# Kernel optimization log

Hardware: AMD Instinct MI355X
Metric: run time of the kernel (lower is better)

## Reference

```python
import jax, jax.numpy as jnp
import numpy as np

FILTER_K = 10      # per-class top-K support retention
TAU = 1.0          # temperature
SCALE = 20.0       # prototype logit scale
EPS = 1e-12


def _normalize(x, axis=-1):
    n = jnp.linalg.norm(x, axis=axis, keepdims=True)
    return x / jnp.maximum(n, EPS)


def _entropy(logits):
    p = jax.nn.softmax(logits, axis=1)
    return -(p * jax.nn.log_softmax(logits, axis=1)).sum(axis=1)


def _quantile(x, q):
    # linear-interpolation quantile (matches torch.quantile default)
    s = jnp.sort(x)
    n = x.shape[0]
    pos = q * (n - 1)
    lo = jnp.floor(pos).astype(jnp.int32)
    hi = jnp.minimum(lo + 1, n - 1)
    frac = pos - lo.astype(x.dtype)
    return s[lo] * (1.0 - frac) + s[hi] * frac


def setup_inputs() -> dict:
    key = jax.random.key(0)
    k1, k2, k3, k4, k5 = jax.random.split(key, 5)
    B, D, C = 65536, 512, 50
    feat = jax.random.normal(k1, (B, D), jnp.float32)
    logits_raw = jax.random.normal(k2, (B, C), jnp.float32)
    logits_aug = jax.random.normal(k3, (B, C), jnp.float32)
    W = jax.random.normal(k4, (C, D), jnp.float32) * 0.05  # classifier weight
    b = jax.random.normal(k5, (C,), jnp.float32) * 0.05    # classifier bias
    return {"feat": feat, "logits_raw": logits_raw, "logits_aug": logits_aug, "W": W, "b": b}


def reference(feat, logits_raw, logits_aug, W, b):
    C, D = W.shape
    # --- warmup memory initialized from classifier weights (as in __init__) ---
    wl = W @ W.T + b                       # (C, C)
    p0 = jax.nn.softmax(wl, axis=1)
    lab0 = jnp.argmax(wl, axis=1)          # (C,)
    ent0 = _entropy(wl)
    conf0 = p0.max(axis=1)

    # --- online batch stats ---
    logits = feat @ W.T + b                # (B, C)
    p = jax.nn.softmax(logits, axis=1)
    yhat = jnp.argmax(logits, axis=1)
    ent = _entropy(logits)
    pmax = p.max(axis=1)

    # dynamic entropy-quantile threshold (ent_thresh=None path)
    m = ent.mean()
    dyn_q = jnp.where(m >= 0.45, 0.25, jnp.where(m >= 0.38, 0.3, 0.4))
    thr = _quantile(ent, dyn_q)
    mask = ent <= thr
    # dual-view consistency gate
    mask &= jnp.argmax(logits_raw, axis=1) == jnp.argmax(logits_aug, axis=1)
    # confidence gate
    conf_thr = jnp.where(m >= 0.45, 0.72, 0.62)
    mask &= pmax >= conf_thr

    # --- grown support memory (warmup + accepted batch samples), static shape + valid mask ---
    supports = jnp.concatenate([W, feat], axis=0)          # (C+B, D)
    lab_idx = jnp.concatenate([lab0, yhat], axis=0)        # (C+B,)
    ents = jnp.concatenate([ent0, ent], axis=0)
    conf = jnp.concatenate([conf0, pmax], axis=0)
    valid = jnp.concatenate([jnp.ones((C,), bool), mask], axis=0)

    # --- per-class top-K lowest-entropy pruning (vectorized over classes) ---
    cls_mask = (lab_idx[None, :] == jnp.arange(C)[:, None]) & valid[None, :]  # (C, C+B)
    masked_ent = jnp.where(cls_mask, ents[None, :], jnp.inf)
    order = jnp.argsort(masked_ent, axis=1)
    ranks = jnp.argsort(order, axis=1)                     # rank of each entry within its class
    keep = (cls_mask & (ranks < FILTER_K)).any(axis=0)     # (C+B,)

    # --- confidence-weighted centroids + cosine-sim classification ---
    S = _normalize(supports)
    onehot = jax.nn.one_hot(lab_idx, C, dtype=supports.dtype)
    lab_w = onehot * jnp.maximum(conf, 1e-6)[:, None] * keep[:, None].astype(supports.dtype)
    denom = jnp.maximum(lab_w.sum(axis=0, keepdims=True), EPS)
    centroids = _normalize((lab_w / denom).T @ S)          # (C, D)
    sim = _normalize(feat) @ centroids.T                   # (B, C)
    return SCALE * sim / max(TAU, 1e-6)
```

## Files before the change

### kernel.cpp

```cpp
#include <hip/hip_runtime.h>
#include <math.h>

constexpr int BN = 65536;
constexpr int DK = 512;
constexpr int CN = 50;
constexpr int FILTK = 10;
constexpr int BR = 64;
constexpr int KC = 32;
constexpr int AS = 36;
constexpr int BS = 68;
constexpr int SELB = 64;

constexpr int W_SC     = 0;
constexpr int W_H1     = 64;
constexpr int W_H2LO   = 2112;
constexpr int W_H2HI   = 4160;
constexpr int W_H3LO   = 6208;
constexpr int W_H3HI   = 7232;
constexpr int ZERO_WORDS = 8256;
constexpr int W_ENT    = ZERO_WORDS;
constexpr int W_PMAX   = W_ENT  + BN;
constexpr int W_YHAT   = W_PMAX + BN;
constexpr int W_CONS   = W_YHAT + BN;
constexpr int W_NORM   = W_CONS + BN;
constexpr int W_LAB0   = W_NORM + BN;
constexpr int W_ENT0   = W_LAB0 + 64;
constexpr int W_CONF0  = W_ENT0 + 64;
constexpr int W_WNORM  = W_CONF0 + 64;
constexpr int LE_CAP   = BN + 64;
constexpr int W_LECLS  = W_WNORM + 64;
constexpr int W_LEENT  = W_LECLS  + LE_CAP;
constexpr int W_LECONF = W_LEENT  + LE_CAP;
constexpr int W_LEORD  = W_LECONF + LE_CAP;
constexpr int W_LESRC  = W_LEORD  + LE_CAP;
constexpr int W_LEW    = W_LESRC  + LE_CAP;
constexpr int W_CENT   = W_LEW    + LE_CAP;

struct Scalars {
    float    sum_ent;
    float    mean;
    float    conf_thr;
    float    frac;
    int      klo;
    int      khi;
    unsigned prefix_lo;
    unsigned rank_lo;
    unsigned prefix_hi;
    unsigned rank_hi;
    float    thr;
    unsigned cnt;
    unsigned done1, done2, done3;
};

__device__ __forceinline__ unsigned fkey(float f) {
    unsigned u = __float_as_uint(f);
    return (u & 0x80000000u) ? ~u : (u | 0x80000000u);
}
__device__ __forceinline__ float funkey(unsigned u) {
    return (u & 0x80000000u) ? __uint_as_float(u & 0x7fffffffu) : __uint_as_float(~u);
}

__global__ void init_kernel(const float* __restrict__ W, const float* __restrict__ bias,
                            int* __restrict__ lab0, float* __restrict__ ent0,
                            float* __restrict__ conf0, float* __restrict__ wnorm,
                            unsigned* __restrict__ wsz) {
    if (blockIdx.x >= CN) {
        for (int i = (blockIdx.x - CN) * 64 + threadIdx.x; i < ZERO_WORDS; i += 128)
            wsz[i] = 0u;
        return;
    }
    __shared__ float wrow[DK];
    const int i = blockIdx.x, l = threadIdx.x;
    float4 v0 = *(const float4*)(W + i * DK + l * 4);
    float4 v1 = *(const float4*)(W + i * DK + 256 + l * 4);
    *(float4*)(wrow + l * 4) = v0;
    *(float4*)(wrow + 256 + l * 4) = v1;
    float sq = v0.x*v0.x + v0.y*v0.y + v0.z*v0.z + v0.w*v0.w
             + v1.x*v1.x + v1.y*v1.y + v1.z*v1.z + v1.w*v1.w;
    #pragma unroll
    for (int m = 1; m < 64; m <<= 1) sq += __shfl_xor(sq, m);
    if (l == 0) wnorm[i] = sqrtf(sq);
    __syncthreads();

    float dot = -INFINITY;
    int   ai  = 0x7fffffff;
    if (l < CN) {
        const float* wj = W + l * DK;
        float d2 = 0.f;
        for (int d = 0; d < DK; d += 4) {
            float4 a  = *(const float4*)(wrow + d);
            float4 b4 = *(const float4*)(wj + d);
            d2 = fmaf(a.x, b4.x, fmaf(a.y, b4.y, fmaf(a.z, b4.z, fmaf(a.w, b4.w, d2))));
        }
        dot = d2 + bias[l];
        ai  = l;
    }
    float mx = dot; int am = ai;
    #pragma unroll
    for (int m = 32; m >= 1; m >>= 1) {
        float o = __shfl_xor(mx, m); int oi = __shfl_xor(am, m);
        if (o > mx || (o == mx && oi < am)) { mx = o; am = oi; }
    }
    float e = 0.f, te = 0.f;
    if (l < CN) { e = expf(dot - mx); te = e * (dot - mx); }
    #pragma unroll
    for (int m = 1; m < 64; m <<= 1) { e += __shfl_xor(e, m); te += __shfl_xor(te, m); }
    if (l == 0) {
        lab0[i]  = am;
        ent0[i]  = logf(e) - te / e;
        conf0[i] = 1.f / e;
    }
}

template <int MODE>
__global__ __launch_bounds__(256) void gemm_kernel(
        const float* __restrict__ A, const float* __restrict__ Bm,
        const float* __restrict__ bias,
        float* __restrict__ ent, float* __restrict__ pmaxA,
        int* __restrict__ yhat, float* __restrict__ rnorm,
        const float* __restrict__ in_norm, float* __restrict__ outp,
        const float* __restrict__ lraw, const float* __restrict__ laug,
        unsigned* __restrict__ consp, Scalars* sc) {
    __shared__ float smem[BR * AS + KC * BS];
    float* Af = smem;
    float* Bw = smem + BR * AS;
    const int t = threadIdx.x;
    const int tx = t & 15, ty = t >> 4;
    const int row0 = blockIdx.x * BR;
    const int srow = t >> 3, sf4 = t & 7;

    if (MODE == 0 && t < BR) {
        int r = row0 + t;
        const float* rp = lraw + r * CN;
        const float* ap = laug + r * CN;
        float m1 = rp[0]; int a1 = 0;
        float m2 = ap[0]; int a2 = 0;
        for (int j = 1; j < CN; j++) {
            float v1 = rp[j]; if (v1 > m1) { m1 = v1; a1 = j; }
            float v2 = ap[j]; if (v2 > m2) { m2 = v2; a2 = j; }
        }
        consp[r] = (a1 == a2) ? 1u : 0u;
    }

    float acc[4][4];
    #pragma unroll
    for (int q = 0; q < 4; q++)
        #pragma unroll
        for (int p = 0; p < 4; p++) acc[q][p] = 0.f;
    float sq0 = 0.f, sq1 = 0.f;

    for (int k0 = 0; k0 < DK; k0 += KC) {
        __syncthreads();
        float4 va0 = *(const float4*)(A + (row0 + srow) * DK + k0 + sf4 * 4);
        float4 va1 = *(const float4*)(A + (row0 + srow + 32) * DK + k0 + sf4 * 4);
        *(float4*)(Af + srow * AS + sf4 * 4) = va0;
        *(float4*)(Af + (srow + 32) * AS + sf4 * 4) = va1;
        if (MODE == 0) {
            sq0 += va0.x*va0.x + va0.y*va0.y + va0.z*va0.z + va0.w*va0.w;
            sq1 += va1.x*va1.x + va1.y*va1.y + va1.z*va1.z + va1.w*va1.w;
        }
        #pragma unroll
        for (int h = 0; h < 2; h++) {
            int c = (t >> 3) + h * 32;
            float4 vb = make_float4(0.f, 0.f, 0.f, 0.f);
            if (c < CN) vb = *(const float4*)(Bm + c * DK + k0 + sf4 * 4);
            Bw[(sf4 * 4 + 0) * BS + c] = vb.x;
            Bw[(sf4 * 4 + 1) * BS + c] = vb.y;
            Bw[(sf4 * 4 + 2) * BS + c] = vb.z;
            Bw[(sf4 * 4 + 3) * BS + c] = vb.w;
        }
        __syncthreads();
        #pragma unroll
        for (int kk = 0; kk < KC; kk += 4) {
            float4 a[4], bb[4];
            #pragma unroll
            for (int q = 0; q < 4; q++) a[q] = *(const float4*)(Af + (ty * 4 + q) * AS + kk);
            #pragma unroll
            for (int j = 0; j < 4; j++) bb[j] = *(const float4*)(Bw + (kk + j) * BS + tx * 4);
            #pragma unroll
            for (int q = 0; q < 4; q++) {
                float aq[4] = {a[q].x, a[q].y, a[q].z, a[q].w};
                #pragma unroll
                for (int j = 0; j < 4; j++) {
                    acc[q][0] = fmaf(aq[j], bb[j].x, acc[q][0]);
                    acc[q][1] = fmaf(aq[j], bb[j].y, acc[q][1]);
                    acc[q][2] = fmaf(aq[j], bb[j].z, acc[q][2]);
                    acc[q][3] = fmaf(aq[j], bb[j].w, acc[q][3]);
                }
            }
        }
    }

    if (MODE == 0) {
        float s0 = sq0, s1 = sq1;
        #pragma unroll
        for (int m = 1; m < 8; m <<= 1) { s0 += __shfl_xor(s0, m); s1 += __shfl_xor(s1, m); }
        if (sf4 == 0) { rnorm[row0 + srow] = sqrtf(s0); rnorm[row0 + srow + 32] = sqrtf(s1); }
        __syncthreads();
        float* L = smem;
        #pragma unroll
        for (int q = 0; q < 4; q++) {
            int r = ty * 4 + q;
            #pragma unroll
            for (int p = 0; p < 4; p++) {
                int c = tx * 4 + p;
                if (c < CN) L[r * 52 + c] = acc[q][p] + bias[c];
            }
        }
        __syncthreads();
        if (t < BR) {
            const float* Lr = L + t * 52;
            float mx = Lr[0]; int am = 0;
            for (int j = 1; j < CN; j++) { float v = Lr[j]; if (v > mx) { mx = v; am = j; } }
            float s = 0.f, tt = 0.f;
            for (int j = 0; j < CN; j++) {
                float d = Lr[j] - mx;
                float e = expf(d);
                s += e; tt += e * d;
            }
            float ev = logf(s) - tt / s;
            ent  [row0 + t] = ev;
            pmaxA[row0 + t] = 1.f / s;
            yhat [row0 + t] = am;
            float es = ev;
            #pragma unroll
            for (int m = 1; m < 64; m <<= 1) es += __shfl_xor(es, m);
            if (t == 0) atomicAdd(&sc->sum_ent, es);
        }
    } else {
        #pragma unroll
        for (int q = 0; q < 4; q++) {
            int r = row0 + ty * 4 + q;
            float sc2 = 20.f / fmaxf(in_norm[r], 1e-12f);
            #pragma unroll
            for (int p = 0; p < 4; p++) {
                int c = tx * 4 + p;
                if (c < CN) outp[r * CN + c] = acc[q][p] * sc2;
            }
        }
    }
}


__global__ __launch_bounds__(256) void sel1_kernel(const float* __restrict__ ent,
                                                   unsigned* __restrict__ H1, Scalars* sc) {
    __shared__ unsigned h[2048];
    __shared__ unsigned part[256];
    __shared__ int last;
    const int t = threadIdx.x;
    for (int b = t; b < 2048; b += 256) h[b] = 0u;
    __syncthreads();
    const int lo = blockIdx.x * (BN / SELB), hi = lo + (BN / SELB);
    for (int i = lo + t; i < hi; i += 256)
        atomicAdd(&h[fkey(ent[i]) >> 21], 1u);
    __syncthreads();
    for (int b = t; b < 2048; b += 256) if (h[b]) atomicAdd(&H1[b], h[b]);
    __threadfence();
    if (t == 0) last = (atomicAdd(&sc->done1, 1u) == SELB - 1) ? 1 : 0;
    __syncthreads();
    if (!last) return;

    for (int b = t; b < 2048; b += 256) h[b] = atomicAdd(&H1[b], 0u);
    __syncthreads();
    unsigned ps = 0;
    #pragma unroll
    for (int j = 0; j < 8; j++) ps += h[t * 8 + j];
    part[t] = ps;
    __syncthreads();
    if (t == 0) {
        float m = sc->sum_ent / (float)BN;
        sc->mean = m;
        float q = (m >= 0.45f) ? 0.25f : ((m >= 0.38f) ? 0.30f : 0.40f);
        sc->conf_thr = (m >= 0.45f) ? 0.72f : 0.62f;
        float pos = q * (float)(BN - 1);
        float flo = floorf(pos);
        sc->frac = pos - flo;
        int klo = (int)flo;
        int khi = klo + 1; if (khi > BN - 1) khi = BN - 1;
        sc->klo = klo; sc->khi = khi;
        for (int pass = 0; pass < 2; pass++) {
            unsigned k = (pass == 0) ? (unsigned)klo : (unsigned)khi;
            unsigned cum = 0; int c = 0;
            for (; c < 255; c++) { unsigned pc = part[c]; if (cum + pc > k) break; cum += pc; }
            int b = c * 8;
            for (; b < c * 8 + 7; b++) { unsigned hb = h[b]; if (cum + hb > k) break; cum += hb; }
            if (pass == 0) { sc->prefix_lo = (unsigned)b; sc->rank_lo = k - cum; }
            else           { sc->prefix_hi = (unsigned)b; sc->rank_hi = k - cum; }
        }
    }
}

__global__ __launch_bounds__(256) void sel2_kernel(const float* __restrict__ ent,
                                                   unsigned* __restrict__ HLO, unsigned* __restrict__ HHI,
                                                   Scalars* sc) {
    __shared__ unsigned hlo[2048], hhi[2048];
    __shared__ unsigned plo_s[256], phi_s[256];
    __shared__ int last;
    const int t = threadIdx.x;
    const unsigned plo = sc->prefix_lo, phi = sc->prefix_hi;
    for (int b = t; b < 2048; b += 256) { hlo[b] = 0u; hhi[b] = 0u; }
    __syncthreads();
    const int lo = blockIdx.x * (BN / SELB), hi = lo + (BN / SELB);
    for (int i = lo + t; i < hi; i += 256) {
        unsigned u = fkey(ent[i]);
        unsigned d1 = u >> 21, d2 = (u >> 10) & 2047u;
        if (d1 == plo) atomicAdd(&hlo[d2], 1u);
        if (d1 == phi) atomicAdd(&hhi[d2], 1u);
    }
    __syncthreads();
    for (int b = t; b < 2048; b += 256) {
        if (hlo[b]) atomicAdd(&HLO[b], hlo[b]);
        if (hhi[b]) atomicAdd(&HHI[b], hhi[b]);
    }
    __threadfence();
    if (t == 0) last = (atomicAdd(&sc->done2, 1u) == SELB - 1) ? 1 : 0;
    __syncthreads();
    if (!last) return;

    for (int b = t; b < 2048; b += 256) { hlo[b] = atomicAdd(&HLO[b], 0u); hhi[b] = atomicAdd(&HHI[b], 0u); }
    __syncthreads();
    unsigned pl = 0, ph = 0;
    #pragma unroll
    for (int j = 0; j < 8; j++) { pl += hlo[t * 8 + j]; ph += hhi[t * 8 + j]; }
    plo_s[t] = pl; phi_s[t] = ph;
    __syncthreads();
    if (t == 0) {
        {
            unsigned k = sc->rank_lo, cum = 0; int c = 0;
            for (; c < 255; c++) { unsigned pc = plo_s[c]; if (cum + pc > k) break; cum += pc; }
            int b = c * 8;
            for (; b < c * 8 + 7; b++) { unsigned hb = hlo[b]; if (cum + hb > k) break; cum += hb; }
            sc->prefix_lo = (plo << 11) | (unsigned)b; sc->rank_lo = k - cum;
        }
        {
            unsigned k = sc->rank_hi, cum = 0; int c = 0;
            for (; c < 255; c++) { unsigned pc = phi_s[c]; if (cum + pc > k) break; cum += pc; }
            int b = c * 8;
            for (; b < c * 8 + 7; b++) { unsigned hb = hhi[b]; if (cum + hb > k) break; cum += hb; }
            sc->prefix_hi = (phi << 11) | (unsigned)b; sc->rank_hi = k - cum;
        }
    }
}

__global__ __launch_bounds__(256) void sel3_kernel(const float* __restrict__ ent,
                                                   unsigned* __restrict__ HLO, unsigned* __restrict__ HHI,
                                                   Scalars* sc) {
    __shared__ unsigned hlo[1024], hhi[1024];
    __shared__ unsigned plo_s[256], phi_s[256];
    __shared__ int last;
    const int t = threadIdx.x;
    const unsigned plo = sc->prefix_lo, phi = sc->prefix_hi;
    for (int b = t; b < 1024; b += 256) { hlo[b] = 0u; hhi[b] = 0u; }
    __syncthreads();
    const int lo = blockIdx.x * (BN / SELB), hi = lo + (BN / SELB);
    for (int i = lo + t; i < hi; i += 256) {
        unsigned u = fkey(ent[i]);
        unsigned p22 = u >> 10, d3 = u & 1023u;
        if (p22 == plo) atomicAdd(&hlo[d3], 1u);
        if (p22 == phi) atomicAdd(&hhi[d3], 1u);
    }
    __syncthreads();
    for (int b = t; b < 1024; b += 256) {
        if (hlo[b]) atomicAdd(&HLO[b], hlo[b]);
        if (hhi[b]) atomicAdd(&HHI[b], hhi[b]);
    }
    __threadfence();
    if (t == 0) last = (atomicAdd(&sc->done3, 1u) == SELB - 1) ? 1 : 0;
    __syncthreads();
    if (!last) return;

    for (int b = t; b < 1024; b += 256) { hlo[b] = atomicAdd(&HLO[b], 0u); hhi[b] = atomicAdd(&HHI[b], 0u); }
    __syncthreads();
    unsigned pl = 0, ph = 0;
    #pragma unroll
    for (int j = 0; j < 4; j++) { pl += hlo[t * 4 + j]; ph += hhi[t * 4 + j]; }
    plo_s[t] = pl; phi_s[t] = ph;
    __syncthreads();
    if (t == 0) {
        float vlo, vhi;
        {
            unsigned k = sc->rank_lo, cum = 0; int c = 0;
            for (; c < 255; c++) { unsigned pc = plo_s[c]; if (cum + pc > k) break; cum += pc; }
            int b = c * 4;
            for (; b < c * 4 + 3; b++) { unsigned hb = hlo[b]; if (cum + hb > k) break; cum += hb; }
            vlo = funkey((plo << 10) | (unsigned)b);
        }
        {
            unsigned k = sc->rank_hi, cum = 0; int c = 0;
            for (; c < 255; c++) { unsigned pc = phi_s[c]; if (cum + pc > k) break; cum += pc; }
            int b = c * 4;
            for (; b < c * 4 + 3; b++) { unsigned hb = hhi[b]; if (cum + hb > k) break; cum += hb; }
            vhi = funkey((phi << 10) | (unsigned)b);
        }
        sc->thr = vlo * (1.f - sc->frac) + vhi * sc->frac;
    }
}

__global__ __launch_bounds__(256) void compact_kernel(
        const float* __restrict__ ent, const float* __restrict__ pmaxA,
        const int* __restrict__ yhat, const unsigned* __restrict__ cons,
        const int* __restrict__ lab0, const float* __restrict__ ent0,
        const float* __restrict__ conf0, Scalars* sc,
        int* le_cls, float* le_ent, float* le_conf, int* le_ord, int* le_src) {
    int i = blockIdx.x * blockDim.x + threadIdx.x;
    if (i < CN) {
        le_cls[i] = lab0[i]; le_ent[i] = ent0[i]; le_conf[i] = conf0[i];
        le_ord[i] = i; le_src[i] = i;
    }
    if (i >= BN) return;
    bool m = (ent[i] <= sc->thr) && (cons[i] != 0u) && (pmaxA[i] >= sc->conf_thr);
    if (m) {
        int pos = (int)atomicAdd(&sc->cnt, 1u);
        int e = CN + pos;
        le_cls[e] = yhat[i]; le_ent[e] = ent[i]; le_conf[e] = pmaxA[i];
        le_ord[e] = CN + i;  le_src[e] = i;
    }
}

__global__ __launch_bounds__(256) void tail_kernel(
        const Scalars* sc, const int* __restrict__ le_cls,
        const float* __restrict__ le_ent, const float* __restrict__ le_conf,
        const int* __restrict__ le_ord, const int* __restrict__ le_src,
        float* __restrict__ le_w,
        const float* __restrict__ W, const float* __restrict__ feat,
        const float* __restrict__ wnorm, const float* __restrict__ rnorm,
        float* __restrict__ cent) {
    __shared__ float cacc[CN * DK];
    const int t = threadIdx.x;
    const int M = CN + (int)sc->cnt;

    for (int e = t; e < M; e += 256) {
        int c = le_cls[e]; float v = le_ent[e]; int o = le_ord[e];
        int cnt = 0;
        for (int e2 = 0; e2 < M && cnt < FILTK; e2++) {
            if (le_cls[e2] == c) {
                float v2 = le_ent[e2];
                if (v2 < v || (v2 == v && le_ord[e2] < o)) cnt++;
            }
        }
        le_w[e] = (cnt < FILTK) ? fmaxf(le_conf[e], 1e-6f) : 0.f;
    }
    for (int d = t; d < CN * DK; d += 256) cacc[d] = 0.f;
    __syncthreads();

    for (int e = 0; e < M; e++) {
        float w = le_w[e];
        if (w <= 0.f) continue;
        int src = le_src[e];
        const float* rowp = (e < CN) ? (W + src * DK) : (feat + (size_t)src * DK);
        float nrm = (e < CN) ? wnorm[src] : rnorm[src];
        float k = w / fmaxf(nrm, 1e-12f);
        float* cp = cacc + le_cls[e] * DK;
        #pragma unroll
        for (int j = 0; j < 2; j++) cp[t + j * 256] += k * rowp[t + j * 256];
    }
    __syncthreads();

    const int w64 = t >> 6, l = t & 63;
    for (int c = w64; c < CN; c += 4) {
        float s = 0.f;
        #pragma unroll
        for (int j = 0; j < 8; j++) { float v = cacc[c * DK + l + j * 64]; s = fmaf(v, v, s); }
        #pragma unroll
        for (int m = 1; m < 64; m <<= 1) s += __shfl_xor(s, m);
        float inv = 1.f / fmaxf(sqrtf(s), 1e-12f);
        #pragma unroll
        for (int j = 0; j < 8; j++) cent[c * DK + l + j * 64] = cacc[c * DK + l + j * 64] * inv;
    }
}

extern "C" void kernel_launch(void* const* d_in, const int* in_sizes, int n_in,
                              void* d_out, int out_size, void* d_ws, size_t ws_size,
                              hipStream_t stream) {
    const float* feat = (const float*)d_in[0];
    const float* lraw = (const float*)d_in[1];
    const float* laug = (const float*)d_in[2];
    const float* W    = (const float*)d_in[3];
    const float* bias = (const float*)d_in[4];
    float* out = (float*)d_out;

    unsigned* wsw    = (unsigned*)d_ws;
    Scalars*  sc     = (Scalars*)(wsw + W_SC);
    unsigned* H1     = wsw + W_H1;
    unsigned* H2LO   = wsw + W_H2LO;
    unsigned* H2HI   = wsw + W_H2HI;
    unsigned* H3LO   = wsw + W_H3LO;
    unsigned* H3HI   = wsw + W_H3HI;
    float*    ent    = (float*)(wsw + W_ENT);
    float*    pmaxA  = (float*)(wsw + W_PMAX);
    int*      yhat   = (int*)(wsw + W_YHAT);
    unsigned* cons   = wsw + W_CONS;
    float*    rnorm  = (float*)(wsw + W_NORM);
    int*      lab0   = (int*)(wsw + W_LAB0);
    float*    ent0   = (float*)(wsw + W_ENT0);
    float*    conf0  = (float*)(wsw + W_CONF0);
    float*    wnorm  = (float*)(wsw + W_WNORM);
    int*      le_cls = (int*)(wsw + W_LECLS);
    float*    le_ent = (float*)(wsw + W_LEENT);
    float*    le_conf= (float*)(wsw + W_LECONF);
    int*      le_ord = (int*)(wsw + W_LEORD);
    int*      le_src = (int*)(wsw + W_LESRC);
    float*    le_w   = (float*)(wsw + W_LEW);
    float*    cent   = (float*)(wsw + W_CENT);

    init_kernel<<<CN + 2, 64, 0, stream>>>(W, bias, lab0, ent0, conf0, wnorm, wsw);
    gemm_kernel<0><<<BN / BR, 256, 0, stream>>>(feat, W, bias, ent, pmaxA, yhat, rnorm,
                                                nullptr, nullptr, lraw, laug, cons, sc);
    sel1_kernel<<<SELB, 256, 0, stream>>>(ent, H1, sc);
    sel2_kernel<<<SELB, 256, 0, stream>>>(ent, H2LO, H2HI, sc);
    sel3_kernel<<<SELB, 256, 0, stream>>>(ent, H3LO, H3HI, sc);
    compact_kernel<<<BN / 256, 256, 0, stream>>>(ent, pmaxA, yhat, cons, lab0, ent0, conf0, sc,
                                                 le_cls, le_ent, le_conf, le_ord, le_src);
    tail_kernel<<<1, 256, 0, stream>>>(sc, le_cls, le_ent, le_conf, le_ord, le_src, le_w,
                                       W, feat, wnorm, rnorm, cent);
    gemm_kernel<1><<<BN / BR, 256, 0, stream>>>(feat, cent, nullptr, nullptr, nullptr, nullptr,
                                                nullptr, rnorm, out, nullptr, nullptr, nullptr, sc);
}
```

Measured before the change: 431.1 us.

## Use split-bf16 MFMA for both GEMMs and parallelize centroid tail per class

Both feature GEMMs move from FP32 FMA SIMT tiling to MFMA 16x16x32 bf16 instructions. Each operand is split into high and low bf16 parts and three products are taken to keep near-fp32 accuracy. The classifier and centroid weights are pre-packed into MFMA fragment layout, in init and in the new tail kernel. The single-block tail kernel, with its O(M^2) rank scan, is replaced by a 64-block per-class kernel that gathers each class's entries into shared memory. The consistency argmax moves into the GEMM epilogue. Risks include a fixed per-class cap of 6144 entries and a small numerical deviation from the split-bf16 products.

```diff
diff --git a/kernel.cpp b/kernel.cpp
--- a/kernel.cpp
+++ b/kernel.cpp
@@ -5,11 +5,13 @@
 constexpr int DK = 512;
 constexpr int CN = 50;
 constexpr int FILTK = 10;
-constexpr int BR = 64;
-constexpr int KC = 32;
-constexpr int AS = 36;
-constexpr int BS = 68;
+constexpr int MB = 128;
+constexpr int NKS = DK / 32;
 constexpr int SELB = 64;
+constexpr int CAP = 6144;
+
+typedef __attribute__((ext_vector_type(8))) short short8;
+typedef __attribute__((ext_vector_type(4))) float f4;
 
 constexpr int W_SC     = 0;
 constexpr int W_H1     = 64;
@@ -18,7 +20,11 @@
 constexpr int W_H3LO   = 6208;
 constexpr int W_H3HI   = 7232;
 constexpr int ZERO_WORDS = 8256;
-constexpr int W_ENT    = ZERO_WORDS;
+constexpr int W_WFH    = 8256;
+constexpr int W_WFL    = W_WFH + 16384;
+constexpr int W_CFH    = W_WFL + 16384;
+constexpr int W_CFL    = W_CFH + 16384;
+constexpr int W_ENT    = W_CFL + 16384;
 constexpr int W_PMAX   = W_ENT  + BN;
 constexpr int W_YHAT   = W_PMAX + BN;
 constexpr int W_CONS   = W_YHAT + BN;
@@ -33,8 +39,6 @@
 constexpr int W_LECONF = W_LEENT  + LE_CAP;
 constexpr int W_LEORD  = W_LECONF + LE_CAP;
 constexpr int W_LESRC  = W_LEORD  + LE_CAP;
-constexpr int W_LEW    = W_LESRC  + LE_CAP;
-constexpr int W_CENT   = W_LEW    + LE_CAP;
 
 struct Scalars {
     float    sum_ent;
@@ -60,23 +64,63 @@
     return (u & 0x80000000u) ? __uint_as_float(u & 0x7fffffffu) : __uint_as_float(~u);
 }
 
+__device__ __forceinline__ short bf16h(float x) {
+    unsigned u = __float_as_uint(x);
+    return (short)((u + 0x7fffu + ((u >> 16) & 1u)) >> 16);
+}
+__device__ __forceinline__ float bf16tof(short h) {
+    return __uint_as_float(((unsigned)(unsigned short)h) << 16);
+}
+__device__ __forceinline__ void cvt8(const float* a, short8& h, short8& l) {
+    #pragma unroll
+    for (int j = 0; j < 8; j++) {
+        short hh = bf16h(a[j]);
+        h[j] = hh;
+        l[j] = bf16h(a[j] - bf16tof(hh));
+    }
+}
+__device__ __forceinline__ int fragidx(int ks, int n, int q, int j) {
+    return ks * 2048 + (n >> 4) * 512 + ((n & 15) + 16 * q) * 8 + j;
+}
+
 __global__ void init_kernel(const float* __restrict__ W, const float* __restrict__ bias,
                             int* __restrict__ lab0, float* __restrict__ ent0,
                             float* __restrict__ conf0, float* __restrict__ wnorm,
-                            unsigned* __restrict__ wsz) {
-    if (blockIdx.x >= CN) {
-        for (int i = (blockIdx.x - CN) * 64 + threadIdx.x; i < ZERO_WORDS; i += 128)
-            wsz[i] = 0u;
+                            unsigned* __restrict__ wsz,
+                            short* __restrict__ wfh, short* __restrict__ wfl) {
+    const int b = blockIdx.x, l = threadIdx.x;
+    if (b >= 64) {
+        for (int i = (b - 64) * 64 + l; i < ZERO_WORDS; i += 128) wsz[i] = 0u;
         return;
     }
+    {
+        int ks = l >> 2, q = l & 3;
+        int dst = fragidx(ks, b, q, 0);
+        if (b < CN) {
+            const float* wp = W + b * DK + l * 8;
+            f4 x = *(const f4*)wp, y = *(const f4*)(wp + 4);
+            float a8[8] = {x[0], x[1], x[2], x[3], y[0], y[1], y[2], y[3]};
+            short8 h, lo2; cvt8(a8, h, lo2);
+            *(short8*)(wfh + dst) = h;
+            *(short8*)(wfl + dst) = lo2;
+        } else {
+            short8 z; 
+            #pragma unroll
+            for (int j = 0; j < 8; j++) z[j] = 0;
+            *(short8*)(wfh + dst) = z;
+            *(short8*)(wfl + dst) = z;
+        }
+    }
+    if (b >= CN) return;
+
     __shared__ float wrow[DK];
-    const int i = blockIdx.x, l = threadIdx.x;
-    float4 v0 = *(const float4*)(W + i * DK + l * 4);
-    float4 v1 = *(const float4*)(W + i * DK + 256 + l * 4);
-    *(float4*)(wrow + l * 4) = v0;
-    *(float4*)(wrow + 256 + l * 4) = v1;
-    float sq = v0.x*v0.x + v0.y*v0.y + v0.z*v0.z + v0.w*v0.w
-             + v1.x*v1.x + v1.y*v1.y + v1.z*v1.z + v1.w*v1.w;
+    const int i = b;
+    f4 v0 = *(const f4*)(W + i * DK + l * 4);
+    f4 v1 = *(const f4*)(W + i * DK + 256 + l * 4);
+    *(f4*)(wrow + l * 4) = v0;
+    *(f4*)(wrow + 256 + l * 4) = v1;
+    float sq = v0[0]*v0[0] + v0[1]*v0[1] + v0[2]*v0[2] + v0[3]*v0[3]
+             + v1[0]*v1[0] + v1[1]*v1[1] + v1[2]*v1[2] + v1[3]*v1[3];
     #pragma unroll
     for (int m = 1; m < 64; m <<= 1) sq += __shfl_xor(sq, m);
     if (l == 0) wnorm[i] = sqrtf(sq);
@@ -88,9 +132,9 @@
         const float* wj = W + l * DK;
         float d2 = 0.f;
         for (int d = 0; d < DK; d += 4) {
-            float4 a  = *(const float4*)(wrow + d);
-            float4 b4 = *(const float4*)(wj + d);
-            d2 = fmaf(a.x, b4.x, fmaf(a.y, b4.y, fmaf(a.z, b4.z, fmaf(a.w, b4.w, d2))));
+            f4 a = *(const f4*)(wrow + d);
+            f4 b4 = *(const f4*)(wj + d);
+            d2 = fmaf(a[0], b4[0], fmaf(a[1], b4[1], fmaf(a[2], b4[2], fmaf(a[3], b4[3], d2))));
         }
         dot = d2 + bias[l];
         ai  = l;
@@ -114,103 +158,83 @@
 
 template <int MODE>
 __global__ __launch_bounds__(256) void gemm_kernel(
-        const float* __restrict__ A, const float* __restrict__ Bm,
+        const float* __restrict__ feat,
+        const short* __restrict__ bfh, const short* __restrict__ bfl,
         const float* __restrict__ bias,
         float* __restrict__ ent, float* __restrict__ pmaxA,
         int* __restrict__ yhat, float* __restrict__ rnorm,
-        const float* __restrict__ in_norm, float* __restrict__ outp,
         const float* __restrict__ lraw, const float* __restrict__ laug,
-        unsigned* __restrict__ consp, Scalars* sc) {
-    __shared__ float smem[BR * AS + KC * BS];
-    float* Af = smem;
-    float* Bw = smem + BR * AS;
+        unsigned* __restrict__ consp, Scalars* sc, float* __restrict__ outp) {
+    constexpr int LSZ = (MODE == 0) ? MB * 65 : 4;
+    __shared__ float L[LSZ];
     const int t = threadIdx.x;
-    const int tx = t & 15, ty = t >> 4;
-    const int row0 = blockIdx.x * BR;
-    const int srow = t >> 3, sf4 = t & 7;
-
-    if (MODE == 0 && t < BR) {
-        int r = row0 + t;
-        const float* rp = lraw + r * CN;
-        const float* ap = laug + r * CN;
-        float m1 = rp[0]; int a1 = 0;
-        float m2 = ap[0]; int a2 = 0;
-        for (int j = 1; j < CN; j++) {
-            float v1 = rp[j]; if (v1 > m1) { m1 = v1; a1 = j; }
-            float v2 = ap[j]; if (v2 > m2) { m2 = v2; a2 = j; }
-        }
-        consp[r] = (a1 == a2) ? 1u : 0u;
-    }
-
-    float acc[4][4];
-    #pragma unroll
-    for (int q = 0; q < 4; q++)
-        #pragma unroll
-        for (int p = 0; p < 4; p++) acc[q][p] = 0.f;
-    float sq0 = 0.f, sq1 = 0.f;
-
-    for (int k0 = 0; k0 < DK; k0 += KC) {
+    const int w = t >> 6, lane = t & 63, m = lane & 15, q = lane >> 4;
+    const int rb = blockIdx.x * MB + w * 32;
+
+    f4 acc[2][4];
+    #pragma unroll
+    for (int mt = 0; mt < 2; mt++)
+        #pragma unroll
+        for (int nt = 0; nt < 4; nt++) acc[mt][nt] = (f4){0.f, 0.f, 0.f, 0.f};
+    float sq[2] = {0.f, 0.f};
+
+    for (int ks = 0; ks < NKS; ks++) {
+        short8 ah[2], al[2];
+        #pragma unroll
+        for (int mt = 0; mt < 2; mt++) {
+            const float* ap = feat + (size_t)(rb + mt * 16 + m) * DK + ks * 32 + q * 8;
+            f4 x = *(const f4*)ap;
+            f4 y = *(const f4*)(ap + 4);
+            float a8[8] = {x[0], x[1], x[2], x[3], y[0], y[1], y[2], y[3]};
+            if (MODE == 0) {
+                sq[mt] += x[0]*x[0] + x[1]*x[1] + x[2]*x[2] + x[3]*x[3]
+                        + y[0]*y[0] + y[1]*y[1] + y[2]*y[2] + y[3]*y[3];
+            }
+            cvt8(a8, ah[mt], al[mt]);
+        }
+        short8 bh[4], bl[4];
+        #pragma unroll
+        for (int nt = 0; nt < 4; nt++) {
+            int off = ks * 2048 + nt * 512 + lane * 8;
+            bh[nt] = *(const short8*)(bfh + off);
+            bl[nt] = *(const short8*)(bfl + off);
+        }
+        #pragma unroll
+        for (int mt = 0; mt < 2; mt++)
+            #pragma unroll
+            for (int nt = 0; nt < 4; nt++) {
+                acc[mt][nt] = __builtin_amdgcn_mfma_f32_16x16x32_bf16(ah[mt], bh[nt], acc[mt][nt], 0, 0, 0);
+                acc[mt][nt] = __builtin_amdgcn_mfma_f32_16x16x32_bf16(al[mt], bh[nt], acc[mt][nt], 0, 0, 0);
+                acc[mt][nt] = __builtin_amdgcn_mfma_f32_16x16x32_bf16(ah[mt], bl[nt], acc[mt][nt], 0, 0, 0);
+            }
+    }
+
+    if (MODE == 0) {
+        #pragma unroll
+        for (int mt = 0; mt < 2; mt++) {
+            float s = sq[mt];
+            s += __shfl_xor(s, 16);
+            s += __shfl_xor(s, 32);
+            if (q == 0) rnorm[rb + mt * 16 + m] = sqrtf(s);
+        }
+        float bc[4];
+        #pragma unroll
+        for (int nt = 0; nt < 4; nt++) { int c = nt * 16 + m; bc[nt] = (c < CN) ? bias[c] : 0.f; }
+        #pragma unroll
+        for (int mt = 0; mt < 2; mt++)
+            #pragma unroll
+            for (int nt = 0; nt < 4; nt++)
+                #pragma unroll
+                for (int r = 0; r < 4; r++) {
+                    int row = w * 32 + mt * 16 + q * 4 + r;
+                    L[row * 65 + nt * 16 + m] = acc[mt][nt][r] + bc[nt];
+                }
         __syncthreads();
-        float4 va0 = *(const float4*)(A + (row0 + srow) * DK + k0 + sf4 * 4);
-        float4 va1 = *(const float4*)(A + (row0 + srow + 32) * DK + k0 + sf4 * 4);
-        *(float4*)(Af + srow * AS + sf4 * 4) = va0;
-        *(float4*)(Af + (srow + 32) * AS + sf4 * 4) = va1;
-        if (MODE == 0) {
-            sq0 += va0.x*va0.x + va0.y*va0.y + va0.z*va0.z + va0.w*va0.w;
-            sq1 += va1.x*va1.x + va1.y*va1.y + va1.z*va1.z + va1.w*va1.w;
-        }
-        #pragma unroll
-        for (int h = 0; h < 2; h++) {
-            int c = (t >> 3) + h * 32;
-            float4 vb = make_float4(0.f, 0.f, 0.f, 0.f);
-            if (c < CN) vb = *(const float4*)(Bm + c * DK + k0 + sf4 * 4);
-            Bw[(sf4 * 4 + 0) * BS + c] = vb.x;
-            Bw[(sf4 * 4 + 1) * BS + c] = vb.y;
-            Bw[(sf4 * 4 + 2) * BS + c] = vb.z;
-            Bw[(sf4 * 4 + 3) * BS + c] = vb.w;
-        }
-        __syncthreads();
-        #pragma unroll
-        for (int kk = 0; kk < KC; kk += 4) {
-            float4 a[4], bb[4];
-            #pragma unroll
-            for (int q = 0; q < 4; q++) a[q] = *(const float4*)(Af + (ty * 4 + q) * AS + kk);
-            #pragma unroll
-            for (int j = 0; j < 4; j++) bb[j] = *(const float4*)(Bw + (kk + j) * BS + tx * 4);
-            #pragma unroll
-            for (int q = 0; q < 4; q++) {
-                float aq[4] = {a[q].x, a[q].y, a[q].z, a[q].w};
-                #pragma unroll
-                for (int j = 0; j < 4; j++) {
-                    acc[q][0] = fmaf(aq[j], bb[j].x, acc[q][0]);
-                    acc[q][1] = fmaf(aq[j], bb[j].y, acc[q][1]);
-                    acc[q][2] = fmaf(aq[j], bb[j].z, acc[q][2]);
-                    acc[q][3] = fmaf(aq[j], bb[j].w, acc[q][3]);
-                }
-            }
-        }
-    }
-
-    if (MODE == 0) {
-        float s0 = sq0, s1 = sq1;
-        #pragma unroll
-        for (int m = 1; m < 8; m <<= 1) { s0 += __shfl_xor(s0, m); s1 += __shfl_xor(s1, m); }
-        if (sf4 == 0) { rnorm[row0 + srow] = sqrtf(s0); rnorm[row0 + srow + 32] = sqrtf(s1); }
-        __syncthreads();
-        float* L = smem;
-        #pragma unroll
-        for (int q = 0; q < 4; q++) {
-            int r = ty * 4 + q;
-            #pragma unroll
-            for (int p = 0; p < 4; p++) {
-                int c = tx * 4 + p;
-                if (c < CN) L[r * 52 + c] = acc[q][p] + bias[c];
-            }
-        }
-        __syncthreads();
-        if (t < BR) {
-            const float* Lr = L + t * 52;
+        if (t < MB) {
+            int grow = blockIdx.x * MB + t;
+            const float* Lr = L + t * 65;
             float mx = Lr[0]; int am = 0;
+            #pragma unroll 10
             for (int j = 1; j < CN; j++) { float v = Lr[j]; if (v > mx) { mx = v; am = j; } }
             float s = 0.f, tt = 0.f;
             for (int j = 0; j < CN; j++) {
@@ -219,28 +243,39 @@
                 s += e; tt += e * d;
             }
             float ev = logf(s) - tt / s;
-            ent  [row0 + t] = ev;
-            pmaxA[row0 + t] = 1.f / s;
-            yhat [row0 + t] = am;
+            ent  [grow] = ev;
+            pmaxA[grow] = 1.f / s;
+            yhat [grow] = am;
+            const float* rp  = lraw + (size_t)grow * CN;
+            const float* apg = laug + (size_t)grow * CN;
+            float m1 = rp[0];  int a1 = 0;
+            float m2 = apg[0]; int a2 = 0;
+            #pragma unroll 10
+            for (int j = 1; j < CN; j++) {
+                float v1 = rp[j];  if (v1 > m1) { m1 = v1; a1 = j; }
+                float v2 = apg[j]; if (v2 > m2) { m2 = v2; a2 = j; }
+            }
+            consp[grow] = (a1 == a2) ? 1u : 0u;
             float es = ev;
             #pragma unroll
-            for (int m = 1; m < 64; m <<= 1) es += __shfl_xor(es, m);
-            if (t == 0) atomicAdd(&sc->sum_ent, es);
+            for (int mk = 1; mk < 64; mk <<= 1) es += __shfl_xor(es, mk);
+            if ((t & 63) == 0) atomicAdd(&sc->sum_ent, es);
         }
     } else {
         #pragma unroll
-        for (int q = 0; q < 4; q++) {
-            int r = row0 + ty * 4 + q;
-            float sc2 = 20.f / fmaxf(in_norm[r], 1e-12f);
+        for (int mt = 0; mt < 2; mt++)
             #pragma unroll
-            for (int p = 0; p < 4; p++) {
-                int c = tx * 4 + p;
-                if (c < CN) outp[r * CN + c] = acc[q][p] * sc2;
+            for (int r = 0; r < 4; r++) {
+                int grow = rb + mt * 16 + q * 4 + r;
+                float s = 20.f / fmaxf(rnorm[grow], 1e-12f);
+                #pragma unroll
+                for (int nt = 0; nt < 4; nt++) {
+                    int c = nt * 16 + m;
+                    if (c < CN) outp[(size_t)grow * CN + c] = acc[mt][nt][r] * s;
+                }
             }
-        }
-    }
-}
-
+    }
+}
 
 __global__ __launch_bounds__(256) void sel1_kernel(const float* __restrict__ ent,
                                                    unsigned* __restrict__ H1, Scalars* sc) {
@@ -417,55 +452,74 @@
     }
 }
 
-__global__ __launch_bounds__(256) void tail_kernel(
+__global__ __launch_bounds__(256) void tail2_kernel(
         const Scalars* sc, const int* __restrict__ le_cls,
         const float* __restrict__ le_ent, const float* __restrict__ le_conf,
         const int* __restrict__ le_ord, const int* __restrict__ le_src,
-        float* __restrict__ le_w,
         const float* __restrict__ W, const float* __restrict__ feat,
         const float* __restrict__ wnorm, const float* __restrict__ rnorm,
-        float* __restrict__ cent) {
-    __shared__ float cacc[CN * DK];
-    const int t = threadIdx.x;
+        short* __restrict__ cfh, short* __restrict__ cfl) {
+    const int c = blockIdx.x, t = threadIdx.x;
+    if (c >= CN) {
+        for (int idx = t; idx < 512; idx += 256) {
+            int ks = idx >> 5, rem = idx & 31, qq = rem >> 3, jj = rem & 7;
+            int dst = fragidx(ks, c, qq, jj);
+            cfh[dst] = 0; cfl[dst] = 0;
+        }
+        return;
+    }
+    __shared__ float sent[CAP];
+    __shared__ int   sord[CAP];
+    __shared__ float sconf[CAP];
+    __shared__ int   ssrc[CAP];
+    __shared__ float wk[CAP];
+    __shared__ float accv[DK];
+    __shared__ float red[4];
+    __shared__ int   mc_s;
+    if (t == 0) mc_s = 0;
+    for (int d = t; d < DK; d += 256) accv[d] = 0.f;
+    __syncthreads();
     const int M = CN + (int)sc->cnt;
-
     for (int e = t; e < M; e += 256) {
-        int c = le_cls[e]; float v = le_ent[e]; int o = le_ord[e];
-        int cnt = 0;
-        for (int e2 = 0; e2 < M && cnt < FILTK; e2++) {
-            if (le_cls[e2] == c) {
-                float v2 = le_ent[e2];
-                if (v2 < v || (v2 == v && le_ord[e2] < o)) cnt++;
-            }
-        }
-        le_w[e] = (cnt < FILTK) ? fmaxf(le_conf[e], 1e-6f) : 0.f;
-    }
-    for (int d = t; d < CN * DK; d += 256) cacc[d] = 0.f;
-    __syncthreads();
-
-    for (int e = 0; e < M; e++) {
-        float w = le_w[e];
-        if (w <= 0.f) continue;
-        int src = le_src[e];
-        const float* rowp = (e < CN) ? (W + src * DK) : (feat + (size_t)src * DK);
-        float nrm = (e < CN) ? wnorm[src] : rnorm[src];
-        float k = w / fmaxf(nrm, 1e-12f);
-        float* cp = cacc + le_cls[e] * DK;
-        #pragma unroll
-        for (int j = 0; j < 2; j++) cp[t + j * 256] += k * rowp[t + j * 256];
-    }
-    __syncthreads();
-
-    const int w64 = t >> 6, l = t & 63;
-    for (int c = w64; c < CN; c += 4) {
-        float s = 0.f;
-        #pragma unroll
-        for (int j = 0; j < 8; j++) { float v = cacc[c * DK + l + j * 64]; s = fmaf(v, v, s); }
-        #pragma unroll
-        for (int m = 1; m < 64; m <<= 1) s += __shfl_xor(s, m);
-        float inv = 1.f / fmaxf(sqrtf(s), 1e-12f);
-        #pragma unroll
-        for (int j = 0; j < 8; j++) cent[c * DK + l + j * 64] = cacc[c * DK + l + j * 64] * inv;
+        if (le_cls[e] == c) {
+            int i = atomicAdd(&mc_s, 1);
+            if (i < CAP) { sent[i] = le_ent[e]; sord[i] = le_ord[e]; sconf[i] = le_conf[e]; ssrc[i] = le_src[e]; }
+        }
+    }
+    __syncthreads();
+    int mc = min(mc_s, CAP);
+    for (int i = t; i < mc; i += 256) {
+        float v = sent[i]; int o = sord[i]; int r = 0;
+        for (int j = 0; j < mc && r < FILTK; j++)
+            if (sent[j] < v || (sent[j] == v && sord[j] < o)) r++;
+        wk[i] = (r < FILTK) ? fmaxf(sconf[i], 1e-6f) : 0.f;
+    }
+    __syncthreads();
+    for (int i = 0; i < mc; i++) {
+        float wgt = wk[i];
+        if (wgt <= 0.f) continue;
+        int src = ssrc[i];
+        bool warm = sord[i] < CN;
+        const float* rowp = warm ? (W + src * DK) : (feat + (size_t)src * DK);
+        float nr = warm ? wnorm[src] : rnorm[src];
+        float k = wgt / fmaxf(nr, 1e-12f);
+        for (int d = t; d < DK; d += 256) accv[d] += k * rowp[d];
+    }
+    __syncthreads();
+    float s = 0.f;
+    for (int d = t; d < DK; d += 256) { float v = accv[d]; s = fmaf(v, v, s); }
+    #pragma unroll
+    for (int mk = 1; mk < 64; mk <<= 1) s += __shfl_xor(s, mk);
+    if ((t & 63) == 0) red[t >> 6] = s;
+    __syncthreads();
+    float inv = 1.f / fmaxf(sqrtf(red[0] + red[1] + red[2] + red[3]), 1e-12f);
+    for (int k = t; k < DK; k += 256) {
+        float v = accv[k] * inv;
+        short hh = bf16h(v);
+        short ll = bf16h(v - bf16tof(hh));
+        int ks = k >> 5, kk = k & 31, qq = kk >> 3, jj = kk & 7;
+        int dst = fragidx(ks, c, qq, jj);
+        cfh[dst] = hh; cfl[dst] = ll;
     }
 }
 
@@ -486,6 +540,10 @@
     unsigned* H2HI   = wsw + W_H2HI;
     unsigned* H3LO   = wsw + W_H3LO;
     unsigned* H3HI   = wsw + W_H3HI;
+    short*    wfh    = (short*)(wsw + W_WFH);
+    short*    wfl    = (short*)(wsw + W_WFL);
+    short*    cfh    = (short*)(wsw + W_CFH);
+    short*    cfl    = (short*)(wsw + W_CFL);
     float*    ent    = (float*)(wsw + W_ENT);
     float*    pmaxA  = (float*)(wsw + W_PMAX);
     int*      yhat   = (int*)(wsw + W_YHAT);
@@ -500,19 +558,17 @@
     float*    le_conf= (float*)(wsw + W_LECONF);
     int*      le_ord = (int*)(wsw + W_LEORD);
     int*      le_src = (int*)(wsw + W_LESRC);
-    float*    le_w   = (float*)(wsw + W_LEW);
-    float*    cent   = (float*)(wsw + W_CENT);
-
-    init_kernel<<<CN + 2, 64, 0, stream>>>(W, bias, lab0, ent0, conf0, wnorm, wsw);
-    gemm_kernel<0><<<BN / BR, 256, 0, stream>>>(feat, W, bias, ent, pmaxA, yhat, rnorm,
-                                                nullptr, nullptr, lraw, laug, cons, sc);
+
+    init_kernel<<<66, 64, 0, stream>>>(W, bias, lab0, ent0, conf0, wnorm, wsw, wfh, wfl);
+    gemm_kernel<0><<<BN / MB, 256, 0, stream>>>(feat, wfh, wfl, bias, ent, pmaxA, yhat, rnorm,
+                                                lraw, laug, cons, sc, nullptr);
     sel1_kernel<<<SELB, 256, 0, stream>>>(ent, H1, sc);
     sel2_kernel<<<SELB, 256, 0, stream>>>(ent, H2LO, H2HI, sc);
     sel3_kernel<<<SELB, 256, 0, stream>>>(ent, H3LO, H3HI, sc);
     compact_kernel<<<BN / 256, 256, 0, stream>>>(ent, pmaxA, yhat, cons, lab0, ent0, conf0, sc,
                                                  le_cls, le_ent, le_conf, le_ord, le_src);
-    tail_kernel<<<1, 256, 0, stream>>>(sc, le_cls, le_ent, le_conf, le_ord, le_src, le_w,
-                                       W, feat, wnorm, rnorm, cent);
-    gemm_kernel<1><<<BN / BR, 256, 0, stream>>>(feat, cent, nullptr, nullptr, nullptr, nullptr,
-                                                nullptr, rnorm, out, nullptr, nullptr, nullptr, sc);
-}
+    tail2_kernel<<<64, 256, 0, stream>>>(sc, le_cls, le_ent, le_conf, le_ord, le_src,
+                                         W, feat, wnorm, rnorm, cfh, cfl);
+    gemm_kernel<1><<<BN / MB, 256, 0, stream>>>(feat, cfh, cfl, nullptr, nullptr, nullptr, nullptr, rnorm,
+                                                nullptr, nullptr, nullptr, sc, out);
+}
```

New measurement: 345.6 us. -19.8%, faster.
